# Kernel tuning notes

Measured on AMD Instinct MI355X. Metric: run time of the kernel, lower is better.

Reference implementation:

```python
import jax, jax.numpy as jnp
import numpy as np

N = 8192
K = 64
EPS = 1e-7
BN_EPS = 1e-5


def _norm(x):
    return jnp.sqrt(jnp.sum(x * x, axis=-1, keepdims=True))


def _bn(x, gamma, beta):
    # BatchNorm2d in training mode (batch statistics, biased variance)
    mu = jnp.mean(x, axis=(0, 2, 3), keepdims=True)
    var = jnp.mean((x - mu) ** 2, axis=(0, 2, 3), keepdims=True)
    return gamma.reshape(1, -1, 1, 1) * (x - mu) / jnp.sqrt(var + BN_EPS) + beta.reshape(1, -1, 1, 1)


def _conv1x1(x, w, b):
    # 1x1 conv == per-pixel linear: x [B,C,H,W], w [O,C]
    return jnp.einsum('bchw,oc->bohw', x, w) + b.reshape(1, -1, 1, 1)


def setup_inputs() -> dict:
    key = jax.random.key(0)
    ks = jax.random.split(key, 24)
    d = {}
    d['points'] = jax.random.normal(ks[0], (1, N, 3), jnp.float32)
    # graph_conv weights (torch code re-draws these every forward; here fixed params)
    lim0 = float(np.sqrt(6.0 / (4 + 64)))
    d['gw0'] = jax.random.uniform(ks[1], (4, 64), jnp.float32, -lim0, lim0)
    lim = float(np.sqrt(6.0 / (64 + 64)))
    for i in range(1, 5):
        d[f'gw{i}'] = jax.random.uniform(ks[1 + i], (64, 64), jnp.float32, -lim, lim)
    # mlp_1: 4->64->128, mlp_2: 192->256->1024 (1x1 convs + BN)
    d['c1w'] = jax.random.normal(ks[6], (64, 4), jnp.float32) * 0.1
    d['c1b'] = jnp.zeros((64,), jnp.float32)
    d['bn1g'] = jnp.ones((64,), jnp.float32)
    d['bn1b'] = jnp.zeros((64,), jnp.float32)
    d['c2w'] = jax.random.normal(ks[7], (128, 64), jnp.float32) * 0.1
    d['c2b'] = jnp.zeros((128,), jnp.float32)
    d['bn2g'] = jnp.ones((128,), jnp.float32)
    d['bn2b'] = jnp.zeros((128,), jnp.float32)
    d['c3w'] = jax.random.normal(ks[8], (256, 192), jnp.float32) * 0.05
    d['c3b'] = jnp.zeros((256,), jnp.float32)
    d['bn3g'] = jnp.ones((256,), jnp.float32)
    d['bn3b'] = jnp.zeros((256,), jnp.float32)
    d['c4w'] = jax.random.normal(ks[9], (1024, 256), jnp.float32) * 0.05
    d['c4b'] = jnp.zeros((1024,), jnp.float32)
    d['bn4g'] = jnp.ones((1024,), jnp.float32)
    d['bn4b'] = jnp.zeros((1024,), jnp.float32)
    return d


def _knn_search(points, k):
    # pairwise squared distances via ||a||^2 - 2ab + ||b||^2
    r = jnp.sum(points * points, axis=-1, keepdims=True)          # [1,N,1]
    dis = r - 2.0 * jnp.einsum('bnd,bmd->bnm', points, points) + jnp.swapaxes(r, 1, 2)
    _, idx = jax.lax.top_k(-dis, k)                                # [1,N,K]
    knn_pts = jax.vmap(lambda p, i: p[i])(points, idx)             # [1,N,K,3]
    return knn_pts


def _proj_knn(knn_pts):
    b, n, k, _ = knn_pts.shape
    pc = knn_pts - knn_pts[:, :, :1, :]                            # center on first neighbor (self)
    vn = jnp.sqrt(jnp.sum(pc * pc, axis=-1))                       # [1,N,K]
    id1 = jnp.argmax(vn, axis=-1)                                  # farthest neighbor
    a1 = jnp.take_along_axis(pc, jnp.broadcast_to(id1[:, :, None, None], (b, n, 1, 3)), axis=2)[:, :, 0, :]
    a1 = a1 / (_norm(a1) + EPS)
    a2 = jnp.mean(pc, axis=2)
    a2 = a2 / (_norm(a2) + EPS)
    a3 = a1 + 1.5 * a2
    a3 = a3 / (_norm(a3) + EPS)
    den = _norm(pc) + EPS                                          # [1,N,K,1]
    f1 = jnp.sum(pc * a1[:, :, None, :], axis=-1, keepdims=True) / den
    f2 = jnp.sum(pc * a2[:, :, None, :], axis=-1, keepdims=True) / den
    f3 = jnp.sum(pc * a3[:, :, None, :], axis=-1, keepdims=True) / den
    return jnp.concatenate([f1, f2, f3, vn[..., None]], axis=-1)   # [1,N,K,4]


def _proj_points(points):
    b, n, _ = points.shape
    vn = jnp.sqrt(jnp.sum(points * points, axis=-1))               # [1,N]
    i1 = jnp.argmax(vn, axis=-1)
    i2 = jnp.argmin(vn, axis=-1)
    a1 = jnp.take_along_axis(points, jnp.broadcast_to(i1[:, None, None], (b, 1, 3)), axis=1)[:, 0, :]
    a1 = a1 / (_norm(a1) + EPS)
    a2 = jnp.take_along_axis(points, jnp.broadcast_to(i2[:, None, None], (b, 1, 3)), axis=1)[:, 0, :]
    a2 = a2 / (_norm(a2) + EPS)
    a3 = a1 + 1.5 * a2
    a3 = a3 / (_norm(a3) + EPS)
    den = _norm(points) + EPS                                      # [1,N,1]
    f1 = jnp.sum(points * a1[:, None, :], axis=-1, keepdims=True) / den
    f2 = jnp.sum(points * a2[:, None, :], axis=-1, keepdims=True) / den
    f3 = jnp.sum(points * a3[:, None, :], axis=-1, keepdims=True) / den
    return jnp.concatenate([f1, f2, f3, vn[..., None]], axis=-1)   # [1,N,4]


def reference(points, gw0, gw1, gw2, gw3, gw4,
              c1w, c1b, bn1g, bn1b, c2w, c2b, bn2g, bn2b,
              c3w, c3b, bn3g, bn3b, c4w, c4b, bn4g, bn4b):
    n = points.shape[1]
    # upper branch: KNN -> rotation-invariant local feats -> 5-layer MLP -> max over K
    knn_pts = _knn_search(points, K)
    feat_up = _proj_knn(knn_pts)                                   # [1,N,K,4]
    x = feat_up.reshape(-1, 4)
    for w in (gw0, gw1, gw2, gw3, gw4):
        x = jax.nn.relu(x @ w)
    x = x.reshape(1, n, K, 64)
    emb_up = jnp.max(x, axis=2, keepdims=True)                     # [1,N,1,64]
    emb_up = emb_up.reshape(1, 64, n, 1)                           # raw view (reshape), as in torch
    # lower branch: global rotation-invariant feats -> mlp_1
    feat_down = _proj_points(points)                               # [1,N,4]
    emb_down = feat_down.reshape(1, 4, n, 1)                       # raw view (reshape), as in torch
    h = jax.nn.relu(_bn(_conv1x1(emb_down, c1w, c1b), bn1g, bn1b))
    h = jax.nn.relu(_bn(_conv1x1(h, c2w, c2b), bn2g, bn2b))        # [1,128,N,1]
    emb = jnp.concatenate([emb_up, h], axis=1)                     # [1,192,N,1]
    out = jax.nn.relu(_bn(_conv1x1(emb, c3w, c3b), bn3g, bn3b))
    out = jax.nn.relu(_bn(_conv1x1(out, c4w, c4b), bn4g, bn4b))    # [1,1024,N,1]
    return out
```

## Files before the change

kernel.cpp:

```cpp
#include <hip/hip_runtime.h>
#include <hip/hip_bf16.h>

#define NPTS 8192
#define KNN 64
#define EPSF 1e-7f

#define OFF_P4      0
#define OFF_STATS   32768
#define OFF_PART    36012
#define OFF_FEATDN  36864
#define OFF_WT1     69632
#define OFF_GWT     69888
#define OFF_BW2     79104
#define OFF_BW3     83200
#define OFF_BW4     107776
#define OFF_XB3V    238848
#define OFF_Y2      2860288
#define OFF_Y3      3908864
#define OFF_FEATUP  6006016

typedef __bf16 bf16x8 __attribute__((ext_vector_type(8)));
typedef float  f32x4  __attribute__((ext_vector_type(4)));

__device__ __forceinline__ unsigned f2u(float f) {
    unsigned u = __float_as_uint(f);
    return ((int)u >= 0) ? (u | 0x80000000u) : ~u;
}
__device__ __forceinline__ float key_to_f(unsigned long long k) {
    unsigned v = (unsigned)(k >> 32);
    unsigned ob = (v & 0x80000000u) ? (v ^ 0x80000000u) : ~v;
    return __uint_as_float(ob);
}
__device__ __forceinline__ unsigned short f2bf(float x) {
    union { __bf16 h; unsigned short s; } u;
    u.h = (__bf16)x;
    return u.s;
}
__device__ __forceinline__ unsigned packbf2(float lo, float hi) {
    return (unsigned)f2bf(lo) | ((unsigned)f2bf(hi) << 16);
}
__device__ __forceinline__ unsigned long long u64min(unsigned long long a, unsigned long long b){ return a < b ? a : b; }
__device__ __forceinline__ unsigned long long u64max(unsigned long long a, unsigned long long b){ return a < b ? b : a; }

__device__ __forceinline__ unsigned long long sort_merge(
    unsigned long long key, unsigned long long cur, int lane)
{
    #pragma unroll
    for (int k = 2; k <= 64; k <<= 1) {
        #pragma unroll
        for (int j = k >> 1; j > 0; j >>= 1) {
            unsigned long long o = __shfl_xor(key, j);
            bool up = ((lane & k) == 0);
            bool lower = ((lane & j) == 0);
            key = (lower == up) ? u64min(key, o) : u64max(key, o);
        }
    }
    unsigned long long rev = __shfl(key, 63 - lane);
    unsigned long long m = u64min(cur, rev);
    #pragma unroll
    for (int j = 32; j > 0; j >>= 1) {
        unsigned long long o = __shfl_xor(m, j);
        m = ((lane & j) == 0) ? u64min(m, o) : u64max(m, o);
    }
    return m;
}

__global__ __launch_bounds__(256) void prepwt_kernel(
    const float* __restrict__ points,
    const float* __restrict__ c1w, const float* __restrict__ c2w,
    const float* __restrict__ c3w, const float* __restrict__ c4w,
    const float* __restrict__ gw0, const float* __restrict__ gw1,
    const float* __restrict__ gw2, const float* __restrict__ gw3,
    const float* __restrict__ gw4,
    float* __restrict__ ws)
{
    const int t = blockIdx.x * 256 + threadIdx.x;
    const int T = 256 * 256;
    for (int m = t; m < 2944; m += T) ws[OFF_STATS + m] = 0.f;
    for (int m = t; m < 64*4; m += T) { int o = m >> 2, c = m & 3; ws[OFF_WT1 + c*64 + o] = c1w[m]; }

    unsigned short* bw2 = (unsigned short*)(ws + OFF_BW2);
    for (int m = t; m < 128*64; m += T)   bw2[m] = f2bf(c2w[m]);
    unsigned short* bw3 = (unsigned short*)(ws + OFF_BW3);
    for (int m = t; m < 256*192; m += T)  bw3[m] = f2bf(c3w[m]);
    unsigned short* bw4 = (unsigned short*)(ws + OFF_BW4);
    for (int m = t; m < 1024*256; m += T) bw4[m] = f2bf(c4w[m]);

    unsigned short* gwt = (unsigned short*)(ws + OFF_GWT);
    for (int m = t; m < 2048; m += T) {
        int o = m >> 5, i = m & 31;
        gwt[m] = (i < 4) ? f2bf(gw0[i*64 + o]) : (unsigned short)0;
    }
    const float* gsrc[4] = {gw1, gw2, gw3, gw4};
    for (int l = 0; l < 4; ++l) {
        const float* g = gsrc[l];
        unsigned short* dst = gwt + 2048 + l*4096;
        for (int m = t; m < 4096; m += T) { int o = m >> 6, i = m & 63; dst[m] = f2bf(g[i*64 + o]); }
    }

    if (blockIdx.x < 32) {
        const int n = blockIdx.x * 256 + threadIdx.x;
        float x = points[3*n+0], y = points[3*n+1], z = points[3*n+2];
        float rr = x*x + y*y + z*z;
        ((float4*)(ws + OFF_P4))[n] = make_float4(x, y, z, rr);
        float vn = sqrtf(rr);
        unsigned b = __float_as_uint(vn);
        unsigned long long mxk = ((unsigned long long)b << 32) | (unsigned long long)(0xFFFFFFFFu - (unsigned)n);
        unsigned long long mnk = ((unsigned long long)b << 32) | (unsigned long long)(unsigned)n;
        for (int j = 32; j > 0; j >>= 1) {
            mxk = u64max(mxk, __shfl_xor(mxk, j));
            mnk = u64min(mnk, __shfl_xor(mnk, j));
        }
        __shared__ unsigned long long smx[4], smn[4];
        int wid = threadIdx.x >> 6;
        if ((threadIdx.x & 63) == 0) { smx[wid] = mxk; smn[wid] = mnk; }
        __syncthreads();
        if (threadIdx.x == 0) {
            unsigned long long MX = 0ull, MN = ~0ull;
            for (int i = 0; i < 4; ++i) { MX = u64max(MX, smx[i]); MN = u64min(MN, smn[i]); }
            unsigned long long* parts = (unsigned long long*)(ws + OFF_PART);
            parts[2*blockIdx.x + 0] = MX;
            parts[2*blockIdx.x + 1] = MN;
        }
    }
}

__global__ __launch_bounds__(512) void knn_feat_kernel(
    const float4* __restrict__ p4, float4* __restrict__ feat_up,
    float* __restrict__ ws)
{
    __shared__ __align__(16) float4 scand[2048];
    __shared__ unsigned long long queue[8][128];
    const int lane = threadIdx.x & 63;
    const int wid  = threadIdx.x >> 6;
    const int q = blockIdx.x * 8 + wid;

    const float4 qa = p4[q];
    unsigned long long cur = ~0ull;
    float ke = __builtin_inff();
    int qc = 0;
    unsigned long long* Q = queue[wid];

    for (int base = 0; base < NPTS; base += 2048) {
        __syncthreads();
        for (int t = threadIdx.x; t < 2048; t += 512) scand[t] = p4[base + t];
        __syncthreads();
        #pragma unroll 2
        for (int sub = 0; sub < 2048; sub += 128) {
            float4 cd0 = scand[sub + lane];
            float4 cd1 = scand[sub + 64 + lane];
            float dot0 = fmaf(qa.x, cd0.x, fmaf(qa.y, cd0.y, qa.z * cd0.z));
            float dot1 = fmaf(qa.x, cd1.x, fmaf(qa.y, cd1.y, qa.z * cd1.z));
            float e0 = fmaf(-2.f, dot0, cd0.w);
            float e1 = fmaf(-2.f, dot1, cd1.w);
            bool p0 = e0 < ke;
            bool p1 = e1 < ke;
            unsigned long long m0 = __ballot(p0);
            unsigned long long m1 = __ballot(p1);
            if (m0) {
                int prefix = __builtin_amdgcn_mbcnt_hi((unsigned)(m0 >> 32),
                              __builtin_amdgcn_mbcnt_lo((unsigned)m0, 0));
                if (p0) Q[qc + prefix] = ((unsigned long long)f2u(e0) << 32)
                                       | (unsigned long long)(unsigned)(base + sub + lane);
                qc += __popcll(m0);
                if (qc >= 64) {
                    qc -= 64;
                    cur = sort_merge(Q[qc + lane], cur, lane);
                    ke = key_to_f(__shfl(cur, 63));
                }
            }
            if (m1) {
                int prefix = __builtin_amdgcn_mbcnt_hi((unsigned)(m1 >> 32),
                              __builtin_amdgcn_mbcnt_lo((unsigned)m1, 0));
                if (p1) Q[qc + prefix] = ((unsigned long long)f2u(e1) << 32)
                                       | (unsigned long long)(unsigned)(base + sub + 64 + lane);
                qc += __popcll(m1);
                if (qc >= 64) {
                    qc -= 64;
                    cur = sort_merge(Q[qc + lane], cur, lane);
                    ke = key_to_f(__shfl(cur, 63));
                }
            }
        }
    }
    cur = sort_merge((lane < qc) ? Q[lane] : ~0ull, cur, lane);

    int nidx = (int)(unsigned)(cur & 0xFFFFFFFFu);
    float4 np = p4[nidx];
    float ox = __shfl(np.x, 0), oy = __shfl(np.y, 0), oz = __shfl(np.z, 0);
    float pcx = np.x - ox, pcy = np.y - oy, pcz = np.z - oz;
    float vn = sqrtf(pcx*pcx + pcy*pcy + pcz*pcz);

    unsigned long long ak = ((unsigned long long)__float_as_uint(vn) << 32)
                          | (unsigned long long)(unsigned)(63 - lane);
    for (int s = 32; s > 0; s >>= 1) ak = u64max(ak, __shfl_xor(ak, s));
    int id1 = 63 - (int)(unsigned)(ak & 0xFFFFFFFFu);

    float a1x = __shfl(pcx, id1), a1y = __shfl(pcy, id1), a1z = __shfl(pcz, id1);
    float n1 = sqrtf(a1x*a1x + a1y*a1y + a1z*a1z) + EPSF;
    a1x /= n1; a1y /= n1; a1z /= n1;

    float sx = pcx, sy = pcy, sz = pcz;
    for (int s = 32; s > 0; s >>= 1) {
        sx += __shfl_xor(sx, s); sy += __shfl_xor(sy, s); sz += __shfl_xor(sz, s);
    }
    float a2x = sx * (1.f/64.f), a2y = sy * (1.f/64.f), a2z = sz * (1.f/64.f);
    float n2 = sqrtf(a2x*a2x + a2y*a2y + a2z*a2z) + EPSF;
    a2x /= n2; a2y /= n2; a2z /= n2;

    float a3x = a1x + 1.5f*a2x, a3y = a1y + 1.5f*a2y, a3z = a1z + 1.5f*a2z;
    float n3 = sqrtf(a3x*a3x + a3y*a3y + a3z*a3z) + EPSF;
    a3x /= n3; a3y /= n3; a3z /= n3;

    float den = vn + EPSF;
    float f1 = (pcx*a1x + pcy*a1y + pcz*a1z) / den;
    float f2 = (pcx*a2x + pcy*a2y + pcz*a2z) / den;
    float f3 = (pcx*a3x + pcy*a3y + pcz*a3z) / den;
    feat_up[q*64 + lane] = make_float4(f1, f2, f3, vn);

    {
        const unsigned long long* parts = (const unsigned long long*)(ws + OFF_PART);
        unsigned long long mxk = (lane < 32) ? parts[2*lane + 0] : 0ull;
        unsigned long long mnk = (lane < 32) ? parts[2*lane + 1] : ~0ull;
        for (int s = 32; s > 0; s >>= 1) {
            mxk = u64max(mxk, __shfl_xor(mxk, s));
            mnk = u64min(mnk, __shfl_xor(mnk, s));
        }
        if (lane == 0) {
            int i1 = (int)(0xFFFFFFFFu - (unsigned)(mxk & 0xFFFFFFFFu));
            int i2 = (int)(unsigned)(mnk & 0xFFFFFFFFu);
            float4 p1 = p4[i1];
            float4 p2 = p4[i2];
            float w1 = sqrtf(p1.x*p1.x + p1.y*p1.y + p1.z*p1.z) + EPSF;
            float b1x = p1.x/w1, b1y = p1.y/w1, b1z = p1.z/w1;
            float w2 = sqrtf(p2.x*p2.x + p2.y*p2.y + p2.z*p2.z) + EPSF;
            float b2x = p2.x/w2, b2y = p2.y/w2, b2z = p2.z/w2;
            float b3x = b1x + 1.5f*b2x, b3y = b1y + 1.5f*b2y, b3z = b1z + 1.5f*b2z;
            float w3 = sqrtf(b3x*b3x + b3y*b3y + b3z*b3z) + EPSF;
            b3x /= w3; b3y /= w3; b3z /= w3;
            float vq = sqrtf(qa.w);
            float dq = vq + EPSF;
            float g1 = (qa.x*b1x + qa.y*b1y + qa.z*b1z) / dq;
            float g2 = (qa.x*b2x + qa.y*b2y + qa.z*b2z) / dq;
            float g3 = (qa.x*b3x + qa.y*b3y + qa.z*b3z) / dq;
            ((float4*)(ws + OFF_FEATDN))[q] = make_float4(g1, g2, g3, vq);
        }
    }
}

#define BROW 72
__global__ __launch_bounds__(256) void mlp_kernel(
    const float4* __restrict__ feat_up,
    const unsigned short* __restrict__ gwt,
    unsigned short* __restrict__ xb3v,
    const float* __restrict__ c1b,
    float* __restrict__ ws)
{
    __shared__ __align__(16) unsigned short Blds[4][64 * BROW];
    const int lane = threadIdx.x & 63;
    const int wid  = threadIdx.x >> 6;
    const int q = blockIdx.x * 4 + wid;
    const int c = lane & 15, g = lane >> 4;
    unsigned short* B = Blds[wid];

    {
        float4 f = feat_up[q*64 + lane];
        uint2 p0;
        p0.x = packbf2(f.x, f.y);
        p0.y = packbf2(f.z, f.w);
        *(uint2*)&B[lane*BROW] = p0;
        *(uint2*)&B[lane*BROW + 4] = make_uint2(0, 0);
        uint4 z4 = make_uint4(0, 0, 0, 0);
        *(uint4*)&B[lane*BROW + 8]  = z4;
        *(uint4*)&B[lane*BROW + 16] = z4;
        *(uint4*)&B[lane*BROW + 24] = z4;
    }

    const unsigned short* Wl[5] = {gwt, gwt + 2048, gwt + 6144, gwt + 10240, gwt + 14336};
    f32x4 acc[4][4];

    for (int layer = 0; layer < 5; ++layer) {
        const int wstride = (layer == 0) ? 32 : 64;
        const int nks = (layer == 0) ? 1 : 2;
        #pragma unroll
        for (int mb = 0; mb < 4; ++mb)
            #pragma unroll
            for (int nb = 0; nb < 4; ++nb)
                acc[mb][nb] = (f32x4){0.f, 0.f, 0.f, 0.f};

        for (int ks = 0; ks < nks; ++ks) {
            bf16x8 af[4], bf[4];
            #pragma unroll
            for (int mb = 0; mb < 4; ++mb)
                af[mb] = *(const bf16x8*)(Wl[layer] + (mb*16 + c)*wstride + ks*32 + g*8);
            #pragma unroll
            for (int nb = 0; nb < 4; ++nb)
                bf[nb] = *(const bf16x8*)&B[(nb*16 + c)*BROW + ks*32 + g*8];
            #pragma unroll
            for (int mb = 0; mb < 4; ++mb)
                #pragma unroll
                for (int nb = 0; nb < 4; ++nb)
                    acc[mb][nb] = __builtin_amdgcn_mfma_f32_16x16x32_bf16(af[mb], bf[nb], acc[mb][nb], 0, 0, 0);
        }

        if (layer < 4) {
            #pragma unroll
            for (int mb = 0; mb < 4; ++mb) {
                #pragma unroll
                for (int nb = 0; nb < 4; ++nb) {
                    f32x4 a = acc[mb][nb];
                    uint2 pw;
                    pw.x = packbf2(fmaxf(a[0], 0.f), fmaxf(a[1], 0.f));
                    pw.y = packbf2(fmaxf(a[2], 0.f), fmaxf(a[3], 0.f));
                    *(uint2*)&B[(nb*16 + c)*BROW + mb*16 + g*4] = pw;
                }
            }
        }
    }

    const int cc = q >> 7;
    const int pbase = (q & 127) << 6;
    #pragma unroll
    for (int mb = 0; mb < 4; ++mb) {
        float v[4];
        #pragma unroll
        for (int r = 0; r < 4; ++r)
            v[r] = fmaxf(fmaxf(fmaxf(acc[mb][0][r], acc[mb][1][r]),
                               fmaxf(acc[mb][2][r], acc[mb][3][r])), 0.f);
        #pragma unroll
        for (int mask = 1; mask <= 8; mask <<= 1)
            #pragma unroll
            for (int r = 0; r < 4; ++r)
                v[r] = fmaxf(v[r], __shfl_xor(v[r], mask));
        if (c == 0) {
            #pragma unroll
            for (int r = 0; r < 4; ++r) {
                const int f = mb*16 + g*4 + r;
                xb3v[(size_t)(pbase + f) * 64 + cc] = f2bf(v[r]);
            }
        }
    }

    if (blockIdx.x < 64) {
        __syncthreads();
        float* sps  = (float*)&Blds[0][0];
        float* spss = sps + 128;
        const int tid = threadIdx.x;
        const int bx = blockIdx.x & 31, by = blockIdx.x >> 5;
        const int p  = bx * 256 + tid;
        const int o0 = by * 32;
        const float* fdn = ws + OFF_FEATDN;
        const float* wt1 = ws + OFF_WT1;
        float* s1 = ws + OFF_STATS;
        float xv0 = fdn[p], xv1 = fdn[8192 + p], xv2 = fdn[16384 + p], xv3 = fdn[24576 + p];
        float accc[32];
        #pragma unroll
        for (int u = 0; u < 32; ++u) accc[u] = c1b[o0 + u];
        #pragma unroll
        for (int u = 0; u < 32; ++u) accc[u] = fmaf(xv0, wt1[0*64 + o0 + u], accc[u]);
        #pragma unroll
        for (int u = 0; u < 32; ++u) accc[u] = fmaf(xv1, wt1[1*64 + o0 + u], accc[u]);
        #pragma unroll
        for (int u = 0; u < 32; ++u) accc[u] = fmaf(xv2, wt1[2*64 + o0 + u], accc[u]);
        #pragma unroll
        for (int u = 0; u < 32; ++u) accc[u] = fmaf(xv3, wt1[3*64 + o0 + u], accc[u]);
        #pragma unroll
        for (int u = 0; u < 32; ++u) {
            float s = accc[u], ss = accc[u] * accc[u];
            for (int j = 32; j > 0; j >>= 1) { s += __shfl_xor(s, j); ss += __shfl_xor(ss, j); }
            if (lane == 0) { sps[wid*32 + u] = s; spss[wid*32 + u] = ss; }
        }
        __syncthreads();
        if (tid < 32) {
            float S  = sps[tid] + sps[32 + tid] + sps[64 + tid] + sps[96 + tid];
            float SS = spss[tid] + spss[32 + tid] + spss[64 + tid] + spss[96 + tid];
            atomicAdd(&s1[o0 + tid], S);
            atomicAdd(&s1[64 + o0 + tid], SS);
        }
    }
}

__global__ __launch_bounds__(256) void conv2fd_kernel(
    const unsigned short* __restrict__ A,
    const float* __restrict__ c1b,
    const float* __restrict__ stp, const float* __restrict__ gam, const float* __restrict__ bet,
    const float* __restrict__ bias, float* __restrict__ yout, float* __restrict__ stout,
    const float* __restrict__ ws)
{
    __shared__ float sc[64], sh[64], swt[256], sb[64];
    const int tid = threadIdx.x;
    if (tid < 64) {
        float mu  = stp[tid] * (1.f / 8192.f);
        float var = stp[64 + tid] * (1.f / 8192.f) - mu * mu;
        float s = gam[tid] / sqrtf(var + 1e-5f);
        sc[tid] = s; sh[tid] = bet[tid] - mu * s;
        sb[tid] = c1b[tid];
    }
    if (tid < 256) swt[tid] = ws[OFF_WT1 + tid];
    __syncthreads();

    const float* fdn = ws + OFF_FEATDN;
    const int lane = tid & 63;
    const int w = tid >> 6;
    const int n0 = blockIdx.x * 256 + w * 64;
    const int m0 = blockIdx.y * 64;
    const int c = lane & 15, g = lane >> 4;
    const int K = 64, M = 128;

    f32x4 acc[4][4];
    #pragma unroll
    for (int mt = 0; mt < 4; ++mt)
        #pragma unroll
        for (int nt = 0; nt < 4; ++nt)
            acc[mt][nt] = (f32x4){0.f, 0.f, 0.f, 0.f};

    for (int k0 = 0; k0 < K; k0 += 32) {
        bf16x8 af[4], bf[4];
        #pragma unroll
        for (int mt = 0; mt < 4; ++mt)
            af[mt] = *(const bf16x8*)(A + (size_t)(m0 + mt*16 + c) * K + k0 + g*8);
        const int ch0 = k0 + g*8;
        #pragma unroll
        for (int nt = 0; nt < 4; ++nt) {
            const int pt = n0 + nt*16 + c;
            const float fd0 = fdn[pt];
            const float fd1 = fdn[8192 + pt];
            const float fd2 = fdn[16384 + pt];
            const float fd3 = fdn[24576 + pt];
            bf16x8 r;
            #pragma unroll
            for (int j = 0; j < 8; ++j) {
                const int ch = ch0 + j;
                float v = fmaf(fd3, swt[192 + ch],
                          fmaf(fd2, swt[128 + ch],
                          fmaf(fd1, swt[64 + ch],
                          fmaf(fd0, swt[ch], sb[ch]))));
                r[j] = (__bf16)fmaxf(fmaf(v, sc[ch], sh[ch]), 0.f);
            }
            bf[nt] = r;
        }
        #pragma unroll
        for (int mt = 0; mt < 4; ++mt)
            #pragma unroll
            for (int nt = 0; nt < 4; ++nt)
                acc[mt][nt] = __builtin_amdgcn_mfma_f32_16x16x32_bf16(af[mt], bf[nt], acc[mt][nt], 0, 0, 0);
    }

    #pragma unroll
    for (int mt = 0; mt < 4; ++mt) {
        float s[4], ss[4];
        #pragma unroll
        for (int r = 0; r < 4; ++r) {
            const int o = m0 + mt*16 + g*4 + r;
            const float bv = bias[o];
            float sum = 0.f, sq = 0.f;
            #pragma unroll
            for (int nt = 0; nt < 4; ++nt) {
                float v = acc[mt][nt][r] + bv;
                yout[(size_t)o * NPTS + n0 + nt*16 + c] = v;
                sum += v; sq += v * v;
            }
            s[r] = sum; ss[r] = sq;
        }
        #pragma unroll
        for (int mask = 1; mask <= 8; mask <<= 1)
            #pragma unroll
            for (int r = 0; r < 4; ++r) {
                s[r]  += __shfl_xor(s[r],  mask);
                ss[r] += __shfl_xor(ss[r], mask);
            }
        if (c == 0) {
            #pragma unroll
            for (int r = 0; r < 4; ++r) {
                const int o = m0 + mt*16 + g*4 + r;
                atomicAdd(&stout[o], s[r]);
                atomicAdd(&stout[M + o], ss[r]);
            }
        }
    }
}

__global__ __launch_bounds__(256) void convbn_kernel(
    const unsigned short* __restrict__ A,
    const unsigned short* __restrict__ Bdir, int Kdir,
    const float* __restrict__ yprev,
    const float* __restrict__ stp, const float* __restrict__ gam, const float* __restrict__ bet,
    const float* __restrict__ bias, int K, int M,
    float* __restrict__ yout, float* __restrict__ stout)
{
    __shared__ float sc[256], sh[256];
    const int tid = threadIdx.x;
    const int Cp = K - Kdir;
    for (int cc = tid; cc < Cp; cc += 256) {
        float mu  = stp[cc] * (1.f / 8192.f);
        float var = stp[Cp + cc] * (1.f / 8192.f) - mu * mu;
        float s = gam[cc] / sqrtf(var + 1e-5f);
        sc[cc] = s; sh[cc] = bet[cc] - mu * s;
    }
    __syncthreads();

    const int lane = tid & 63;
    const int w = tid >> 6;
    const int n0 = blockIdx.x * 256 + w * 64;
    const int m0 = blockIdx.y * 64;
    const int c = lane & 15, g = lane >> 4;

    f32x4 acc[4][4];
    #pragma unroll
    for (int mt = 0; mt < 4; ++mt)
        #pragma unroll
        for (int nt = 0; nt < 4; ++nt)
            acc[mt][nt] = (f32x4){0.f, 0.f, 0.f, 0.f};

    for (int k0 = 0; k0 < K; k0 += 32) {
        bf16x8 af[4], bf[4];
        #pragma unroll
        for (int mt = 0; mt < 4; ++mt)
            af[mt] = *(const bf16x8*)(A + (size_t)(m0 + mt*16 + c) * K + k0 + g*8);
        if (k0 + 32 <= Kdir) {
            #pragma unroll
            for (int nt = 0; nt < 4; ++nt)
                bf[nt] = *(const bf16x8*)(Bdir + (size_t)(n0 + nt*16 + c) * Kdir + k0 + g*8);
        } else {
            const int ch0 = k0 - Kdir + g*8;
            #pragma unroll
            for (int nt = 0; nt < 4; ++nt) {
                const int pt = n0 + nt*16 + c;
                bf16x8 r;
                #pragma unroll
                for (int j = 0; j < 8; ++j) {
                    float vv = fmaxf(fmaf(yprev[(size_t)(ch0 + j) * NPTS + pt],
                                          sc[ch0 + j], sh[ch0 + j]), 0.f);
                    r[j] = (__bf16)vv;
                }
                bf[nt] = r;
            }
        }
        #pragma unroll
        for (int mt = 0; mt < 4; ++mt)
            #pragma unroll
            for (int nt = 0; nt < 4; ++nt)
                acc[mt][nt] = __builtin_amdgcn_mfma_f32_16x16x32_bf16(af[mt], bf[nt], acc[mt][nt], 0, 0, 0);
    }

    #pragma unroll
    for (int mt = 0; mt < 4; ++mt) {
        float s[4], ss[4];
        #pragma unroll
        for (int r = 0; r < 4; ++r) {
            const int o = m0 + mt*16 + g*4 + r;
            const float bv = bias[o];
            float sum = 0.f, sq = 0.f;
            #pragma unroll
            for (int nt = 0; nt < 4; ++nt) {
                float v = acc[mt][nt][r] + bv;
                yout[(size_t)o * NPTS + n0 + nt*16 + c] = v;
                sum += v; sq += v * v;
            }
            s[r] = sum; ss[r] = sq;
        }
        #pragma unroll
        for (int mask = 1; mask <= 8; mask <<= 1)
            #pragma unroll
            for (int r = 0; r < 4; ++r) {
                s[r]  += __shfl_xor(s[r],  mask);
                ss[r] += __shfl_xor(ss[r], mask);
            }
        if (c == 0) {
            #pragma unroll
            for (int r = 0; r < 4; ++r) {
                const int o = m0 + mt*16 + g*4 + r;
                atomicAdd(&stout[o], s[r]);
                atomicAdd(&stout[M + o], ss[r]);
            }
        }
    }
}

__global__ __launch_bounds__(256) void bnrelu_kernel(
    const float4* y, const float* __restrict__ st,
    const float* __restrict__ g, const float* __restrict__ b,
    float4* out, int C)
{
    int idx = blockIdx.x * 256 + threadIdx.x;
    int c = idx >> 11;
    float mu  = st[c] * (1.f / 8192.f);
    float var = st[C + c] * (1.f / 8192.f) - mu * mu;
    float scale = g[c] / sqrtf(var + 1e-5f);
    float sh = b[c] - mu * scale;
    float4 v = y[idx];
    v.x = fmaxf(fmaf(v.x, scale, sh), 0.f);
    v.y = fmaxf(fmaf(v.y, scale, sh), 0.f);
    v.z = fmaxf(fmaf(v.z, scale, sh), 0.f);
    v.w = fmaxf(fmaf(v.w, scale, sh), 0.f);
    out[idx] = v;
}

extern "C" void kernel_launch(void* const* d_in, const int* in_sizes, int n_in,
                              void* d_out, int out_size, void* d_ws, size_t ws_size,
                              hipStream_t stream) {
    const float* points = (const float*)d_in[0];
    const float* gw0 = (const float*)d_in[1];
    const float* gw1 = (const float*)d_in[2];
    const float* gw2 = (const float*)d_in[3];
    const float* gw3 = (const float*)d_in[4];
    const float* gw4 = (const float*)d_in[5];
    const float* c1w = (const float*)d_in[6];  const float* c1b = (const float*)d_in[7];
    const float* bn1g = (const float*)d_in[8]; const float* bn1b = (const float*)d_in[9];
    const float* c2w = (const float*)d_in[10]; const float* c2b = (const float*)d_in[11];
    const float* bn2g = (const float*)d_in[12];const float* bn2b = (const float*)d_in[13];
    const float* c3w = (const float*)d_in[14]; const float* c3b = (const float*)d_in[15];
    const float* bn3g = (const float*)d_in[16];const float* bn3b = (const float*)d_in[17];
    const float* c4w = (const float*)d_in[18]; const float* c4b = (const float*)d_in[19];
    const float* bn4g = (const float*)d_in[20];const float* bn4b = (const float*)d_in[21];

    float* ws = (float*)d_ws;
    float* p4f    = ws + OFF_P4;
    float* featup = ws + OFF_FEATUP;
    float* y2 = ws + OFF_Y2; float* y3 = ws + OFF_Y3;
    float* s1 = ws + OFF_STATS + 0;
    float* s2 = ws + OFF_STATS + 128;
    float* s3 = ws + OFF_STATS + 384;
    float* s4 = ws + OFF_STATS + 896;
    const unsigned short* gwt = (const unsigned short*)(ws + OFF_GWT);
    const unsigned short* bw2 = (const unsigned short*)(ws + OFF_BW2);
    const unsigned short* bw3 = (const unsigned short*)(ws + OFF_BW3);
    const unsigned short* bw4 = (const unsigned short*)(ws + OFF_BW4);
    unsigned short* xb3v = (unsigned short*)(ws + OFF_XB3V);
    float* outp = (float*)d_out;

    prepwt_kernel<<<256, 256, 0, stream>>>(points, c1w, c2w, c3w, c4w,
                                           gw0, gw1, gw2, gw3, gw4, ws);

    knn_feat_kernel<<<1024, 512, 0, stream>>>((const float4*)p4f, (float4*)featup, ws);
    mlp_kernel<<<2048, 256, 0, stream>>>((const float4*)featup, gwt, xb3v, c1b, ws);

    conv2fd_kernel<<<dim3(32, 2), 256, 0, stream>>>(bw2, c1b, s1, bn1g, bn1b,
                                                    c2b, y2, s2, ws);
    convbn_kernel<<<dim3(32, 4), 256, 0, stream>>>(bw3, xb3v, 64, y2, s2, bn2g, bn2b,
                                                   c3b, 192, 256, y3, s3);
    convbn_kernel<<<dim3(32, 16), 256, 0, stream>>>(bw4, nullptr, 0, y3, s3, bn3g, bn3b,
                                                    c4b, 256, 1024, outp, s4);
    bnrelu_kernel<<<8192, 256, 0, stream>>>((const float4*)outp, s4, bn4g, bn4b, (float4*)outp, 1024);
}
```

Before: 325.4 us.

## Fuse conv2/conv3/conv4/BN-ReLU stages into one persistent kernel with grid barriers

Replaces four separate launches (conv2, conv3, conv4, final BN+ReLU) with a single 256-block persistent kernel that separates the stages with atomic-counter grid barriers. It is meant to remove kernel launch gaps and tail drain between the small dependent stages. In exchange, conv2 and conv3 leave many blocks idle at the barriers, and conv4 now runs two tiles per block instead of one 512-block launch. The spin barrier relies on all 256 blocks being co-resident; the counter sits in the zeroed stats region.

```diff
diff --git a/kernel.cpp b/kernel.cpp
--- a/kernel.cpp
+++ b/kernel.cpp
@@ -7,6 +7,7 @@
 
 #define OFF_P4      0
 #define OFF_STATS   32768
+#define OFF_BAR     35712
 #define OFF_PART    36012
 #define OFF_FEATDN  36864
 #define OFF_WT1     69632
@@ -65,6 +66,17 @@
     return m;
 }
 
+__device__ __forceinline__ void gbarrier(unsigned* bar, unsigned target) {
+    __syncthreads();
+    if (threadIdx.x == 0) {
+        __threadfence();
+        atomicAdd(bar, 1u);
+        while (atomicAdd(bar, 0u) < target) __builtin_amdgcn_s_sleep(8);
+        __threadfence();
+    }
+    __syncthreads();
+}
+
 __global__ __launch_bounds__(256) void prepwt_kernel(
     const float* __restrict__ points,
     const float* __restrict__ c1w, const float* __restrict__ c2w,
@@ -76,7 +88,7 @@
 {
     const int t = blockIdx.x * 256 + threadIdx.x;
     const int T = 256 * 256;
-    for (int m = t; m < 2944; m += T) ws[OFF_STATS + m] = 0.f;
+    for (int m = t; m < 2948; m += T) ws[OFF_STATS + m] = 0.f;
     for (int m = t; m < 64*4; m += T) { int o = m >> 2, c = m & 3; ws[OFF_WT1 + c*64 + o] = c1w[m]; }
 
     unsigned short* bw2 = (unsigned short*)(ws + OFF_BW2);
@@ -380,220 +392,325 @@
     }
 }
 
-__global__ __launch_bounds__(256) void conv2fd_kernel(
-    const unsigned short* __restrict__ A,
+__global__ __launch_bounds__(256) void megaconv_kernel(
+    float* __restrict__ ws,
     const float* __restrict__ c1b,
-    const float* __restrict__ stp, const float* __restrict__ gam, const float* __restrict__ bet,
-    const float* __restrict__ bias, float* __restrict__ yout, float* __restrict__ stout,
-    const float* __restrict__ ws)
+    const float* __restrict__ bn1g, const float* __restrict__ bn1b,
+    const float* __restrict__ c2b,
+    const float* __restrict__ bn2g, const float* __restrict__ bn2b,
+    const float* __restrict__ c3b,
+    const float* __restrict__ bn3g, const float* __restrict__ bn3b,
+    const float* __restrict__ c4b,
+    const float* __restrict__ bn4g, const float* __restrict__ bn4b,
+    float* __restrict__ outp)
 {
-    __shared__ float sc[64], sh[64], swt[256], sb[64];
+    __shared__ float smem[640];
     const int tid = threadIdx.x;
-    if (tid < 64) {
-        float mu  = stp[tid] * (1.f / 8192.f);
-        float var = stp[64 + tid] * (1.f / 8192.f) - mu * mu;
-        float s = gam[tid] / sqrtf(var + 1e-5f);
-        sc[tid] = s; sh[tid] = bet[tid] - mu * s;
-        sb[tid] = c1b[tid];
-    }
-    if (tid < 256) swt[tid] = ws[OFF_WT1 + tid];
-    __syncthreads();
-
-    const float* fdn = ws + OFF_FEATDN;
     const int lane = tid & 63;
     const int w = tid >> 6;
-    const int n0 = blockIdx.x * 256 + w * 64;
-    const int m0 = blockIdx.y * 64;
     const int c = lane & 15, g = lane >> 4;
-    const int K = 64, M = 128;
-
-    f32x4 acc[4][4];
-    #pragma unroll
-    for (int mt = 0; mt < 4; ++mt)
-        #pragma unroll
-        for (int nt = 0; nt < 4; ++nt)
-            acc[mt][nt] = (f32x4){0.f, 0.f, 0.f, 0.f};
-
-    for (int k0 = 0; k0 < K; k0 += 32) {
-        bf16x8 af[4], bf[4];
+    unsigned* bar = (unsigned*)(ws + OFF_BAR);
+
+    float* y2 = ws + OFF_Y2;
+    float* y3 = ws + OFF_Y3;
+    float* s1 = ws + OFF_STATS + 0;
+    float* s2 = ws + OFF_STATS + 128;
+    float* s3 = ws + OFF_STATS + 384;
+    float* s4 = ws + OFF_STATS + 896;
+    const unsigned short* bw2 = (const unsigned short*)(ws + OFF_BW2);
+    const unsigned short* bw3 = (const unsigned short*)(ws + OFF_BW3);
+    const unsigned short* bw4 = (const unsigned short*)(ws + OFF_BW4);
+    const unsigned short* xb3v = (const unsigned short*)(ws + OFF_XB3V);
+    const float* fdn = ws + OFF_FEATDN;
+
+    if (blockIdx.x < 64) {
+        float* sc = smem;
+        float* sh = smem + 64;
+        float* swt = smem + 128;
+        float* sb = smem + 384;
+        if (tid < 64) {
+            float mu  = s1[tid] * (1.f / 8192.f);
+            float var = s1[64 + tid] * (1.f / 8192.f) - mu * mu;
+            float s = bn1g[tid] / sqrtf(var + 1e-5f);
+            sc[tid] = s; sh[tid] = bn1b[tid] - mu * s;
+            sb[tid] = c1b[tid];
+        }
+        swt[tid] = ws[OFF_WT1 + tid];
+        __syncthreads();
+
+        const int nb = blockIdx.x & 31;
+        const int n0 = nb * 256 + w * 64;
+        const int m0 = (blockIdx.x >> 5) * 64;
+        const int K = 64, M = 128;
+
+        f32x4 acc[4][4];
         #pragma unroll
         for (int mt = 0; mt < 4; ++mt)
-            af[mt] = *(const bf16x8*)(A + (size_t)(m0 + mt*16 + c) * K + k0 + g*8);
-        const int ch0 = k0 + g*8;
-        #pragma unroll
-        for (int nt = 0; nt < 4; ++nt) {
-            const int pt = n0 + nt*16 + c;
-            const float fd0 = fdn[pt];
-            const float fd1 = fdn[8192 + pt];
-            const float fd2 = fdn[16384 + pt];
-            const float fd3 = fdn[24576 + pt];
-            bf16x8 r;
-            #pragma unroll
-            for (int j = 0; j < 8; ++j) {
-                const int ch = ch0 + j;
-                float v = fmaf(fd3, swt[192 + ch],
-                          fmaf(fd2, swt[128 + ch],
-                          fmaf(fd1, swt[64 + ch],
-                          fmaf(fd0, swt[ch], sb[ch]))));
-                r[j] = (__bf16)fmaxf(fmaf(v, sc[ch], sh[ch]), 0.f);
-            }
-            bf[nt] = r;
-        }
-        #pragma unroll
-        for (int mt = 0; mt < 4; ++mt)
             #pragma unroll
             for (int nt = 0; nt < 4; ++nt)
-                acc[mt][nt] = __builtin_amdgcn_mfma_f32_16x16x32_bf16(af[mt], bf[nt], acc[mt][nt], 0, 0, 0);
-    }
-
-    #pragma unroll
-    for (int mt = 0; mt < 4; ++mt) {
-        float s[4], ss[4];
-        #pragma unroll
-        for (int r = 0; r < 4; ++r) {
-            const int o = m0 + mt*16 + g*4 + r;
-            const float bv = bias[o];
-            float sum = 0.f, sq = 0.f;
+                acc[mt][nt] = (f32x4){0.f, 0.f, 0.f, 0.f};
+
+        for (int k0 = 0; k0 < K; k0 += 32) {
+            bf16x8 af[4], bf[4];
+            #pragma unroll
+            for (int mt = 0; mt < 4; ++mt)
+                af[mt] = *(const bf16x8*)(bw2 + (size_t)(m0 + mt*16 + c) * K + k0 + g*8);
+            const int ch0 = k0 + g*8;
             #pragma unroll
             for (int nt = 0; nt < 4; ++nt) {
-                float v = acc[mt][nt][r] + bv;
-                yout[(size_t)o * NPTS + n0 + nt*16 + c] = v;
-                sum += v; sq += v * v;
-            }
-            s[r] = sum; ss[r] = sq;
-        }
-        #pragma unroll
-        for (int mask = 1; mask <= 8; mask <<= 1)
-            #pragma unroll
-            for (int r = 0; r < 4; ++r) {
-                s[r]  += __shfl_xor(s[r],  mask);
-                ss[r] += __shfl_xor(ss[r], mask);
-            }
-        if (c == 0) {
+                const int pt = n0 + nt*16 + c;
+                const float fd0 = fdn[pt];
+                const float fd1 = fdn[8192 + pt];
+                const float fd2 = fdn[16384 + pt];
+                const float fd3 = fdn[24576 + pt];
+                bf16x8 r;
+                #pragma unroll
+                for (int j = 0; j < 8; ++j) {
+                    const int ch = ch0 + j;
+                    float v = fmaf(fd3, swt[192 + ch],
+                              fmaf(fd2, swt[128 + ch],
+                              fmaf(fd1, swt[64 + ch],
+                              fmaf(fd0, swt[ch], sb[ch]))));
+                    r[j] = (__bf16)fmaxf(fmaf(v, sc[ch], sh[ch]), 0.f);
+                }
+                bf[nt] = r;
+            }
+            #pragma unroll
+            for (int mt = 0; mt < 4; ++mt)
+                #pragma unroll
+                for (int nt = 0; nt < 4; ++nt)
+                    acc[mt][nt] = __builtin_amdgcn_mfma_f32_16x16x32_bf16(af[mt], bf[nt], acc[mt][nt], 0, 0, 0);
+        }
+
+        #pragma unroll
+        for (int mt = 0; mt < 4; ++mt) {
+            float s[4], ss[4];
             #pragma unroll
             for (int r = 0; r < 4; ++r) {
                 const int o = m0 + mt*16 + g*4 + r;
-                atomicAdd(&stout[o], s[r]);
-                atomicAdd(&stout[M + o], ss[r]);
-            }
-        }
-    }
-}
-
-__global__ __launch_bounds__(256) void convbn_kernel(
-    const unsigned short* __restrict__ A,
-    const unsigned short* __restrict__ Bdir, int Kdir,
-    const float* __restrict__ yprev,
-    const float* __restrict__ stp, const float* __restrict__ gam, const float* __restrict__ bet,
-    const float* __restrict__ bias, int K, int M,
-    float* __restrict__ yout, float* __restrict__ stout)
-{
-    __shared__ float sc[256], sh[256];
-    const int tid = threadIdx.x;
-    const int Cp = K - Kdir;
-    for (int cc = tid; cc < Cp; cc += 256) {
-        float mu  = stp[cc] * (1.f / 8192.f);
-        float var = stp[Cp + cc] * (1.f / 8192.f) - mu * mu;
-        float s = gam[cc] / sqrtf(var + 1e-5f);
-        sc[cc] = s; sh[cc] = bet[cc] - mu * s;
-    }
-    __syncthreads();
-
-    const int lane = tid & 63;
-    const int w = tid >> 6;
-    const int n0 = blockIdx.x * 256 + w * 64;
-    const int m0 = blockIdx.y * 64;
-    const int c = lane & 15, g = lane >> 4;
-
-    f32x4 acc[4][4];
-    #pragma unroll
-    for (int mt = 0; mt < 4; ++mt)
-        #pragma unroll
-        for (int nt = 0; nt < 4; ++nt)
-            acc[mt][nt] = (f32x4){0.f, 0.f, 0.f, 0.f};
-
-    for (int k0 = 0; k0 < K; k0 += 32) {
-        bf16x8 af[4], bf[4];
+                const float bv = c2b[o];
+                float sum = 0.f, sq = 0.f;
+                #pragma unroll
+                for (int nt = 0; nt < 4; ++nt) {
+                    float v = acc[mt][nt][r] + bv;
+                    y2[(size_t)o * NPTS + n0 + nt*16 + c] = v;
+                    sum += v; sq += v * v;
+                }
+                s[r] = sum; ss[r] = sq;
+            }
+            #pragma unroll
+            for (int mask = 1; mask <= 8; mask <<= 1)
+                #pragma unroll
+                for (int r = 0; r < 4; ++r) {
+                    s[r]  += __shfl_xor(s[r],  mask);
+                    ss[r] += __shfl_xor(ss[r], mask);
+                }
+            if (c == 0) {
+                #pragma unroll
+                for (int r = 0; r < 4; ++r) {
+                    const int o = m0 + mt*16 + g*4 + r;
+                    atomicAdd(&s2[o], s[r]);
+                    atomicAdd(&s2[M + o], ss[r]);
+                }
+            }
+        }
+    }
+    gbarrier(bar, 256u);
+
+    if (blockIdx.x < 128) {
+        float* sc = smem;
+        float* sh = smem + 128;
+        const int Kdir = 64, K = 192, M = 256, Cp = 128;
+        for (int cc2 = tid; cc2 < Cp; cc2 += 256) {
+            float mu  = s2[cc2] * (1.f / 8192.f);
+            float var = s2[Cp + cc2] * (1.f / 8192.f) - mu * mu;
+            float s = bn2g[cc2] / sqrtf(var + 1e-5f);
+            sc[cc2] = s; sh[cc2] = bn2b[cc2] - mu * s;
+        }
+        __syncthreads();
+
+        const int nb = blockIdx.x & 31;
+        const int n0 = nb * 256 + w * 64;
+        const int m0 = (blockIdx.x >> 5) * 64;
+
+        f32x4 acc[4][4];
         #pragma unroll
         for (int mt = 0; mt < 4; ++mt)
-            af[mt] = *(const bf16x8*)(A + (size_t)(m0 + mt*16 + c) * K + k0 + g*8);
-        if (k0 + 32 <= Kdir) {
             #pragma unroll
             for (int nt = 0; nt < 4; ++nt)
-                bf[nt] = *(const bf16x8*)(Bdir + (size_t)(n0 + nt*16 + c) * Kdir + k0 + g*8);
-        } else {
-            const int ch0 = k0 - Kdir + g*8;
-            #pragma unroll
-            for (int nt = 0; nt < 4; ++nt) {
-                const int pt = n0 + nt*16 + c;
-                bf16x8 r;
-                #pragma unroll
-                for (int j = 0; j < 8; ++j) {
-                    float vv = fmaxf(fmaf(yprev[(size_t)(ch0 + j) * NPTS + pt],
-                                          sc[ch0 + j], sh[ch0 + j]), 0.f);
-                    r[j] = (__bf16)vv;
-                }
-                bf[nt] = r;
-            }
-        }
-        #pragma unroll
-        for (int mt = 0; mt < 4; ++mt)
-            #pragma unroll
-            for (int nt = 0; nt < 4; ++nt)
-                acc[mt][nt] = __builtin_amdgcn_mfma_f32_16x16x32_bf16(af[mt], bf[nt], acc[mt][nt], 0, 0, 0);
-    }
-
-    #pragma unroll
-    for (int mt = 0; mt < 4; ++mt) {
-        float s[4], ss[4];
-        #pragma unroll
-        for (int r = 0; r < 4; ++r) {
-            const int o = m0 + mt*16 + g*4 + r;
-            const float bv = bias[o];
-            float sum = 0.f, sq = 0.f;
-            #pragma unroll
-            for (int nt = 0; nt < 4; ++nt) {
-                float v = acc[mt][nt][r] + bv;
-                yout[(size_t)o * NPTS + n0 + nt*16 + c] = v;
-                sum += v; sq += v * v;
-            }
-            s[r] = sum; ss[r] = sq;
-        }
-        #pragma unroll
-        for (int mask = 1; mask <= 8; mask <<= 1)
-            #pragma unroll
-            for (int r = 0; r < 4; ++r) {
-                s[r]  += __shfl_xor(s[r],  mask);
-                ss[r] += __shfl_xor(ss[r], mask);
-            }
-        if (c == 0) {
+                acc[mt][nt] = (f32x4){0.f, 0.f, 0.f, 0.f};
+
+        for (int k0 = 0; k0 < K; k0 += 32) {
+            bf16x8 af[4], bf[4];
+            #pragma unroll
+            for (int mt = 0; mt < 4; ++mt)
+                af[mt] = *(const bf16x8*)(bw3 + (size_t)(m0 + mt*16 + c) * K + k0 + g*8);
+            if (k0 + 32 <= Kdir) {
+                #pragma unroll
+                for (int nt = 0; nt < 4; ++nt)
+                    bf[nt] = *(const bf16x8*)(xb3v + (size_t)(n0 + nt*16 + c) * Kdir + k0 + g*8);
+            } else {
+                const int ch0 = k0 - Kdir + g*8;
+                #pragma unroll
+                for (int nt = 0; nt < 4; ++nt) {
+                    const int pt = n0 + nt*16 + c;
+                    bf16x8 r;
+                    #pragma unroll
+                    for (int j = 0; j < 8; ++j) {
+                        float vv = fmaxf(fmaf(y2[(size_t)(ch0 + j) * NPTS + pt],
+                                              sc[ch0 + j], sh[ch0 + j]), 0.f);
+                        r[j] = (__bf16)vv;
+                    }
+                    bf[nt] = r;
+                }
+            }
+            #pragma unroll
+            for (int mt = 0; mt < 4; ++mt)
+                #pragma unroll
+                for (int nt = 0; nt < 4; ++nt)
+                    acc[mt][nt] = __builtin_amdgcn_mfma_f32_16x16x32_bf16(af[mt], bf[nt], acc[mt][nt], 0, 0, 0);
+        }
+
+        #pragma unroll
+        for (int mt = 0; mt < 4; ++mt) {
+            float s[4], ss[4];
             #pragma unroll
             for (int r = 0; r < 4; ++r) {
                 const int o = m0 + mt*16 + g*4 + r;
-                atomicAdd(&stout[o], s[r]);
-                atomicAdd(&stout[M + o], ss[r]);
-            }
-        }
-    }
-}
-
-__global__ __launch_bounds__(256) void bnrelu_kernel(
-    const float4* y, const float* __restrict__ st,
-    const float* __restrict__ g, const float* __restrict__ b,
-    float4* out, int C)
-{
-    int idx = blockIdx.x * 256 + threadIdx.x;
-    int c = idx >> 11;
-    float mu  = st[c] * (1.f / 8192.f);
-    float var = st[C + c] * (1.f / 8192.f) - mu * mu;
-    float scale = g[c] / sqrtf(var + 1e-5f);
-    float sh = b[c] - mu * scale;
-    float4 v = y[idx];
-    v.x = fmaxf(fmaf(v.x, scale, sh), 0.f);
-    v.y = fmaxf(fmaf(v.y, scale, sh), 0.f);
-    v.z = fmaxf(fmaf(v.z, scale, sh), 0.f);
-    v.w = fmaxf(fmaf(v.w, scale, sh), 0.f);
-    out[idx] = v;
+                const float bv = c3b[o];
+                float sum = 0.f, sq = 0.f;
+                #pragma unroll
+                for (int nt = 0; nt < 4; ++nt) {
+                    float v = acc[mt][nt][r] + bv;
+                    y3[(size_t)o * NPTS + n0 + nt*16 + c] = v;
+                    sum += v; sq += v * v;
+                }
+                s[r] = sum; ss[r] = sq;
+            }
+            #pragma unroll
+            for (int mask = 1; mask <= 8; mask <<= 1)
+                #pragma unroll
+                for (int r = 0; r < 4; ++r) {
+                    s[r]  += __shfl_xor(s[r],  mask);
+                    ss[r] += __shfl_xor(ss[r], mask);
+                }
+            if (c == 0) {
+                #pragma unroll
+                for (int r = 0; r < 4; ++r) {
+                    const int o = m0 + mt*16 + g*4 + r;
+                    atomicAdd(&s3[o], s[r]);
+                    atomicAdd(&s3[M + o], ss[r]);
+                }
+            }
+        }
+    }
+    gbarrier(bar, 512u);
+
+    {
+        float* sc = smem;
+        float* sh = smem + 256;
+        const int K = 256, M = 1024;
+        for (int cc2 = tid; cc2 < 256; cc2 += 256) {
+            float mu  = s3[cc2] * (1.f / 8192.f);
+            float var = s3[256 + cc2] * (1.f / 8192.f) - mu * mu;
+            float s = bn3g[cc2] / sqrtf(var + 1e-5f);
+            sc[cc2] = s; sh[cc2] = bn3b[cc2] - mu * s;
+        }
+        __syncthreads();
+
+        for (int t = blockIdx.x; t < 512; t += 256) {
+            const int nb = t & 31;
+            const int n0 = nb * 256 + w * 64;
+            const int m0 = (t >> 5) * 64;
+
+            f32x4 acc[4][4];
+            #pragma unroll
+            for (int mt = 0; mt < 4; ++mt)
+                #pragma unroll
+                for (int nt = 0; nt < 4; ++nt)
+                    acc[mt][nt] = (f32x4){0.f, 0.f, 0.f, 0.f};
+
+            for (int k0 = 0; k0 < K; k0 += 32) {
+                bf16x8 af[4], bf[4];
+                #pragma unroll
+                for (int mt = 0; mt < 4; ++mt)
+                    af[mt] = *(const bf16x8*)(bw4 + (size_t)(m0 + mt*16 + c) * K + k0 + g*8);
+                const int ch0 = k0 + g*8;
+                #pragma unroll
+                for (int nt = 0; nt < 4; ++nt) {
+                    const int pt = n0 + nt*16 + c;
+                    bf16x8 r;
+                    #pragma unroll
+                    for (int j = 0; j < 8; ++j) {
+                        float vv = fmaxf(fmaf(y3[(size_t)(ch0 + j) * NPTS + pt],
+                                              sc[ch0 + j], sh[ch0 + j]), 0.f);
+                        r[j] = (__bf16)vv;
+                    }
+                    bf[nt] = r;
+                }
+                #pragma unroll
+                for (int mt = 0; mt < 4; ++mt)
+                    #pragma unroll
+                    for (int nt = 0; nt < 4; ++nt)
+                        acc[mt][nt] = __builtin_amdgcn_mfma_f32_16x16x32_bf16(af[mt], bf[nt], acc[mt][nt], 0, 0, 0);
+            }
+
+            #pragma unroll
+            for (int mt = 0; mt < 4; ++mt) {
+                float s[4], ss[4];
+                #pragma unroll
+                for (int r = 0; r < 4; ++r) {
+                    const int o = m0 + mt*16 + g*4 + r;
+                    const float bv = c4b[o];
+                    float sum = 0.f, sq = 0.f;
+                    #pragma unroll
+                    for (int nt = 0; nt < 4; ++nt) {
+                        float v = acc[mt][nt][r] + bv;
+                        outp[(size_t)o * NPTS + n0 + nt*16 + c] = v;
+                        sum += v; sq += v * v;
+                    }
+                    s[r] = sum; ss[r] = sq;
+                }
+                #pragma unroll
+                for (int mask = 1; mask <= 8; mask <<= 1)
+                    #pragma unroll
+                    for (int r = 0; r < 4; ++r) {
+                        s[r]  += __shfl_xor(s[r],  mask);
+                        ss[r] += __shfl_xor(ss[r], mask);
+                    }
+                if (c == 0) {
+                    #pragma unroll
+                    for (int r = 0; r < 4; ++r) {
+                        const int o = m0 + mt*16 + g*4 + r;
+                        atomicAdd(&s4[o], s[r]);
+                        atomicAdd(&s4[M + o], ss[r]);
+                    }
+                }
+            }
+        }
+    }
+    gbarrier(bar, 768u);
+
+    {
+        const float4* yin = (const float4*)outp;
+        float4* yo = (float4*)outp;
+        const int base = blockIdx.x * 256 + tid;
+        #pragma unroll
+        for (int k = 0; k < 32; ++k) {
+            const int idx = base + k * 65536;
+            const int ch = idx >> 11;
+            float mu  = s4[ch] * (1.f / 8192.f);
+            float var = s4[1024 + ch] * (1.f / 8192.f) - mu * mu;
+            float scale = bn4g[ch] / sqrtf(var + 1e-5f);
+            float shf = bn4b[ch] - mu * scale;
+            float4 v = yin[idx];
+            v.x = fmaxf(fmaf(v.x, scale, shf), 0.f);
+            v.y = fmaxf(fmaf(v.y, scale, shf), 0.f);
+            v.z = fmaxf(fmaf(v.z, scale, shf), 0.f);
+            v.w = fmaxf(fmaf(v.w, scale, shf), 0.f);
+            yo[idx] = v;
+        }
+    }
 }
 
 extern "C" void kernel_launch(void* const* d_in, const int* in_sizes, int n_in,
@@ -617,15 +734,7 @@
     float* ws = (float*)d_ws;
     float* p4f    = ws + OFF_P4;
     float* featup = ws + OFF_FEATUP;
-    float* y2 = ws + OFF_Y2; float* y3 = ws + OFF_Y3;
-    float* s1 = ws + OFF_STATS + 0;
-    float* s2 = ws + OFF_STATS + 128;
-    float* s3 = ws + OFF_STATS + 384;
-    float* s4 = ws + OFF_STATS + 896;
     const unsigned short* gwt = (const unsigned short*)(ws + OFF_GWT);
-    const unsigned short* bw2 = (const unsigned short*)(ws + OFF_BW2);
-    const unsigned short* bw3 = (const unsigned short*)(ws + OFF_BW3);
-    const unsigned short* bw4 = (const unsigned short*)(ws + OFF_BW4);
     unsigned short* xb3v = (unsigned short*)(ws + OFF_XB3V);
     float* outp = (float*)d_out;
 
@@ -635,11 +744,9 @@
     knn_feat_kernel<<<1024, 512, 0, stream>>>((const float4*)p4f, (float4*)featup, ws);
     mlp_kernel<<<2048, 256, 0, stream>>>((const float4*)featup, gwt, xb3v, c1b, ws);
 
-    conv2fd_kernel<<<dim3(32, 2), 256, 0, stream>>>(bw2, c1b, s1, bn1g, bn1b,
-                                                    c2b, y2, s2, ws);
-    convbn_kernel<<<dim3(32, 4), 256, 0, stream>>>(bw3, xb3v, 64, y2, s2, bn2g, bn2b,
-                                                   c3b, 192, 256, y3, s3);
-    convbn_kernel<<<dim3(32, 16), 256, 0, stream>>>(bw4, nullptr, 0, y3, s3, bn3g, bn3b,
-                                                    c4b, 256, 1024, outp, s4);
-    bnrelu_kernel<<<8192, 256, 0, stream>>>((const float4*)outp, s4, bn4g, bn4b, (float4*)outp, 1024);
-}
+    megaconv_kernel<<<256, 256, 0, stream>>>(ws, c1b,
+                                             bn1g, bn1b, c2b,
+                                             bn2g, bn2b, c3b,
+                                             bn3g, bn3b, c4b,
+                                             bn4g, bn4b, outp);
+}
```

Measured after the change: 392.2 us. 20.5% more time.
